# Performance work log

Measured on AMD Instinct MI355X. Metric: run time of the kernel, lower is better.

The kernel has to match this reference:

```python
import jax, jax.numpy as jnp
import numpy as np

N = 16384      # nodes
E = 524288     # edges (avg degree 32)
D = 128        # node_dim
H = 256        # hidden_dim
C = 10         # num_classes
G = 64         # graphs in batch


def setup_inputs() -> dict:
    key = jax.random.key(0)
    ks = jax.random.split(key, 8)
    x = jax.random.normal(ks[0], (N, D), dtype=jnp.float32)
    edge_index = jax.random.randint(ks[1], (2, E), 0, N)
    batch = jnp.sort(jax.random.randint(ks[2], (N,), 0, G))
    s = 0.05
    W1 = jax.random.normal(ks[3], (D, H), dtype=jnp.float32) * s
    b1 = jnp.zeros((H,), dtype=jnp.float32)
    W2 = jax.random.normal(ks[4], (H, H), dtype=jnp.float32) * s
    b2 = jnp.zeros((H,), dtype=jnp.float32)
    Wc = jax.random.normal(ks[5], (H, C), dtype=jnp.float32) * s
    bc = jnp.zeros((C,), dtype=jnp.float32)
    return {"x": x, "edge_index": edge_index, "batch": batch,
            "W1": W1, "b1": b1, "W2": W2, "b2": b2, "Wc": Wc, "bc": bc}


def _adj_norm(edge_index, n, dtype):
    # dense adjacency with self-loops (duplicates collapse to 1 via .set),
    # symmetric degree normalization D^{-1/2} A D^{-1/2}
    adj = jnp.zeros((n, n), dtype=dtype)
    adj = adj.at[edge_index[0], edge_index[1]].set(1.0)
    diag = jnp.arange(n)
    adj = adj.at[diag, diag].set(1.0)
    deg = jnp.clip(adj.sum(axis=1), 1.0, None)
    dis = deg ** -0.5
    return dis[:, None] * adj * dis[None, :]


def reference(x, edge_index, batch, W1, b1, W2, b2, Wc, bc):
    n = x.shape[0]
    A = _adj_norm(edge_index, n, x.dtype)   # [n, n], same for both layers
    h = jax.nn.relu((A @ x) @ W1 + b1)      # GCN layer 1 + relu
    h = jax.nn.relu((A @ h) @ W2 + b2)      # GCN layer 2 + relu
    pooled = jax.ops.segment_sum(h, batch, num_segments=G)            # [G, H]
    counts = jax.ops.segment_sum(jnp.ones((n,), h.dtype), batch, num_segments=G)
    pooled = pooled / jnp.clip(counts, 1.0, None)[:, None]
    # dropout is identity in eval mode
    return pooled @ Wc + bc                  # [G, C]
```

## Files before the change

### kernel.cpp

```cpp
#include <hip/hip_runtime.h>
#include <hip/hip_bf16.h>
#include <hip/hip_fp16.h>

#define NN 16384
#define EE 524288
#define DDIM 128
#define HDIM 256
#define CDIM 10
#define GG 64
#define MAXD 128
#define WPR 512

typedef _Float16 h8 __attribute__((ext_vector_type(8)));
typedef float f4 __attribute__((ext_vector_type(4)));
typedef unsigned short su8 __attribute__((ext_vector_type(8)));

#define OFF_BM   0ull
#define OFF_Y1H  0ull
#define OFF_H1   8388608ull
#define OFF_Y2H  16777216ull
#define OFF_XH   33554432ull
#define OFF_ELL  37748736ull
#define OFF_DIS  41943040ull
#define OFF_DEG  42008576ull
#define OFF_POOL 42074112ull
#define OFF_CNT  42139648ull
#define OFF_WT1  42205184ull
#define OFF_WT2  42270720ull

__global__ void cvt_f16(const float* __restrict__ in, _Float16* __restrict__ out) {
    int i = (blockIdx.x * blockDim.x + threadIdx.x) * 4;
    float4 v = *(const float4*)(in + i);
    _Float16 o[4] = {(_Float16)v.x, (_Float16)v.y, (_Float16)v.z, (_Float16)v.w};
    *(ushort4*)(out + i) = *(ushort4*)o;
}

__global__ void cvt_wt(const float* __restrict__ W, _Float16* __restrict__ Wt, int K) {
    int i = blockIdx.x * 256 + threadIdx.x;
    int n = i / K, k = i - n * K;
    Wt[i] = (_Float16)W[k * 256 + n];
}

__global__ void zero_selfloop(uint4* p) {
    int i = blockIdx.x * blockDim.x + threadIdx.x;
    int stride = gridDim.x * blockDim.x;
    const int n16 = NN * WPR / 4;
    for (; i < n16; i += stride) {
        uint4 z = make_uint4(0u, 0u, 0u, 0u);
        int r = i >> 7;
        int slot = i & 127;
        int sw = r >> 5;
        if ((sw >> 2) == slot) {
            unsigned bit = 1u << (r & 31);
            int comp = sw & 3;
            if (comp == 0) z.x = bit;
            else if (comp == 1) z.y = bit;
            else if (comp == 2) z.z = bit;
            else z.w = bit;
        }
        p[i] = z;
    }
}

__global__ void zero_f(float* p, int n) {
    int i = blockIdx.x * blockDim.x + threadIdx.x;
    if (i < n) p[i] = 0.0f;
}

__global__ void edge_kernel(const int* __restrict__ ei, unsigned* bm) {
    int e = blockIdx.x * blockDim.x + threadIdx.x;
    if (e < EE) {
        int s = ei[e];
        int d = ei[EE + e];
        atomicOr(&bm[s * WPR + (d >> 5)], 1u << (d & 31));
    }
}

__global__ void extract_kernel(const unsigned* __restrict__ bm,
                               unsigned short* __restrict__ ell, int* __restrict__ deg,
                               float* __restrict__ dis) {
    int gtid = blockIdx.x * blockDim.x + threadIdx.x;
    int row  = gtid >> 6;
    int lane = threadIdx.x & 63;
    if (row >= NN) return;
    const uint4* wp = (const uint4*)(bm + (size_t)row * WPR + lane * 8);
    uint4 a = wp[0];
    uint4 b = wp[1];
    unsigned w[8] = {a.x, a.y, a.z, a.w, b.x, b.y, b.z, b.w};
    int pc = 0;
#pragma unroll
    for (int k = 0; k < 8; k++) pc += __popc(w[k]);
    int pre = pc;
#pragma unroll
    for (int off = 1; off < 64; off <<= 1) {
        int o = __shfl_up(pre, off, 64);
        if (lane >= off) pre += o;
    }
    int total = __shfl(pre, 63, 64);
    pre -= pc;
    int base = row * MAXD;
    int pos = pre;
#pragma unroll
    for (int k = 0; k < 8; k++) {
        unsigned bits = w[k];
        int cbase = lane * 256 + k * 32;
        while (bits) {
            int bit = __ffs(bits) - 1;
            if (pos < MAXD) ell[base + pos] = (unsigned short)(cbase + bit);
            pos++;
            bits &= bits - 1;
        }
    }
    if (lane == 0) {
        deg[row] = total < MAXD ? total : MAXD;
        dis[row] = 1.0f / sqrtf((float)total);
    }
}

__global__ __launch_bounds__(256) void spmm_f16(const _Float16* __restrict__ src,
                                                const unsigned short* __restrict__ ell,
                                                const int* __restrict__ deg,
                                                const float* __restrict__ dis,
                                                _Float16* __restrict__ y, int P) {
    __shared__ int2  scw[MAXD];
    __shared__ float red[8][128];
    const int row  = blockIdx.x;
    const int p    = blockIdx.y;
    const int t    = threadIdx.x;
    const int wv   = t >> 6;
    const int lane = t & 63;
    const int half = lane >> 5;
    const int l32  = lane & 31;
    const int d    = deg[row];
    if (t < MAXD) {
        if (t < d) {
            int c = ell[row * MAXD + t];
            scw[t] = make_int2(c, __float_as_int(dis[c]));
        } else {
            scw[t] = make_int2(0, 0);
        }
    }
    __syncthreads();

    const _Float16* plane = src + (size_t)p * NN * 128;
    float a0 = 0.0f, a1 = 0.0f, a2 = 0.0f, a3 = 0.0f;
#pragma unroll 4
    for (int k = wv * 2 + half; k < d; k += 8) {
        int2 pr = scw[k];
        float wgt = __int_as_float(pr.y);
        ushort4 u = *(const ushort4*)(plane + (size_t)pr.x * 128 + l32 * 4);
        _Float16 f0 = *(_Float16*)&u.x, f1 = *(_Float16*)&u.y;
        _Float16 f2 = *(_Float16*)&u.z, f3 = *(_Float16*)&u.w;
        a0 = fmaf(wgt, (float)f0, a0);
        a1 = fmaf(wgt, (float)f1, a1);
        a2 = fmaf(wgt, (float)f2, a2);
        a3 = fmaf(wgt, (float)f3, a3);
    }
    *(float4*)&red[wv * 2 + half][l32 * 4] = make_float4(a0, a1, a2, a3);
    __syncthreads();
    if (t < 128) {
        float s = 0.0f;
#pragma unroll
        for (int q = 0; q < 8; q++) s += red[q][t];
        y[(size_t)row * (P * 128) + p * 128 + t] = (_Float16)(dis[row] * s);
    }
}

#define ASTR 40
#define BSTR 40

#define MFMA_PROLOG                                                            \
    const int r0 = blockIdx.x * 128;                                           \
    const int c0 = blockIdx.y * 64;                                            \
    const int t = threadIdx.x;                                                 \
    const int lane = t & 63, wv = t >> 6;                                      \
    const int wm = wv >> 1, wn = wv & 1;                                       \
    const int qm = lane & 15, qk = lane >> 4;                                  \
    f4 acc[4][2];                                                              \
    _Pragma("unroll") for (int i = 0; i < 4; i++)                              \
        _Pragma("unroll") for (int j = 0; j < 2; j++)                          \
            acc[i][j] = (f4){0.f, 0.f, 0.f, 0.f};

#define MFMA_KLOOP(Aptr, Wtptr, K)                                             \
    for (int k0 = 0; k0 < K; k0 += 32) {                                       \
        __syncthreads();                                                       \
        {                                                                      \
            int r = t >> 1, ko = (t & 1) * 16;                                 \
            const su8* srcA = (const su8*)(Aptr + (size_t)(r0 + r) * K + k0 + ko); \
            su8 a0 = srcA[0], a1 = srcA[1];                                    \
            *(su8*)&As[r * ASTR + ko]     = a0;                                \
            *(su8*)&As[r * ASTR + ko + 8] = a1;                                \
            int n = t >> 2, ko2 = (t & 3) * 8;                                 \
            *(su8*)&Bs[n * BSTR + ko2] =                                       \
                *(const su8*)(Wtptr + (size_t)(c0 + n) * K + k0 + ko2);        \
        }                                                                      \
        __syncthreads();                                                       \
        h8 bfr[2];                                                             \
        _Pragma("unroll") for (int j = 0; j < 2; j++)                          \
            bfr[j] = *(const h8*)&Bs[(wn * 32 + j * 16 + qm) * BSTR + qk * 8]; \
        _Pragma("unroll") for (int i = 0; i < 4; i++) {                        \
            h8 afr = *(const h8*)&As[(wm * 64 + i * 16 + qm) * ASTR + qk * 8]; \
            _Pragma("unroll") for (int j = 0; j < 2; j++)                      \
                acc[i][j] = __builtin_amdgcn_mfma_f32_16x16x32_f16(            \
                    afr, bfr[j], acc[i][j], 0, 0, 0);                          \
        }                                                                      \
    }

template <int K>
__global__ __launch_bounds__(256) void gemm_mfma_f16(
        const _Float16* __restrict__ A, const _Float16* __restrict__ Wt,
        const float* __restrict__ bias, _Float16* __restrict__ H) {
    __shared__ __align__(16) _Float16 As[128 * ASTR];
    __shared__ __align__(16) _Float16 Bs[64 * BSTR];
    __shared__ __align__(16) _Float16 Cs[128 * 72];
    MFMA_PROLOG
    MFMA_KLOOP(A, Wt, K)

    float bv[2];
#pragma unroll
    for (int j = 0; j < 2; j++) bv[j] = bias[c0 + wn * 32 + j * 16 + qm];
#pragma unroll
    for (int i = 0; i < 4; i++)
#pragma unroll
        for (int j = 0; j < 2; j++) {
            int lc = wn * 32 + j * 16 + qm;
#pragma unroll
            for (int rr = 0; rr < 4; rr++) {
                int lr = wm * 64 + i * 16 + qk * 4 + rr;
                Cs[lr * 72 + lc] = (_Float16)fmaxf(acc[i][j][rr] + bv[j], 0.0f);
            }
        }
    __syncthreads();
    {
        int r = t >> 1, half_ = t & 1;
        const int pl = c0 >> 7;
        const int cw = (c0 & 127) + half_ * 32;
        _Float16* dst = H + (size_t)pl * NN * 128 + (size_t)(r0 + r) * 128 + cw;
        const _Float16* srcc = &Cs[r * 72 + half_ * 32];
#pragma unroll
        for (int q = 0; q < 4; q++)
            *(su8*)(dst + q * 8) = *(const su8*)(srcc + q * 8);
    }
}

#define NG 8
template <int K>
__global__ __launch_bounds__(256) void gemm_mfma_pool(
        const _Float16* __restrict__ A, const _Float16* __restrict__ Wt,
        const float* __restrict__ bias, const int* __restrict__ batch,
        float* __restrict__ pooled) {
    __shared__ __align__(16) _Float16 As[128 * ASTR];
    __shared__ __align__(16) _Float16 Bs[64 * BSTR];
    __shared__ float pools[NG][68];
    __shared__ int sb[128];
    MFMA_PROLOG
    if (t < 128) sb[t] = batch[r0 + t];
    for (int i = t; i < NG * 68; i += 256) ((float*)pools)[i] = 0.0f;
    MFMA_KLOOP(A, Wt, K)

    float bv[2];
#pragma unroll
    for (int j = 0; j < 2; j++) bv[j] = bias[c0 + wn * 32 + j * 16 + qm];
    __syncthreads();
    const int g0 = sb[0];
#pragma unroll
    for (int i = 0; i < 4; i++)
#pragma unroll
        for (int j = 0; j < 2; j++) {
            int lc = wn * 32 + j * 16 + qm;
#pragma unroll
            for (int rr = 0; rr < 4; rr++) {
                int lr = wm * 64 + i * 16 + qk * 4 + rr;
                int gi = min(sb[lr] - g0, NG - 1);
                float v = fmaxf(acc[i][j][rr] + bv[j], 0.0f);
                atomicAdd(&pools[gi][lc], v);
            }
        }
    __syncthreads();
    const int ng = min(sb[127] - g0 + 1, NG);
    for (int i2 = t; i2 < ng * 64; i2 += 256) {
        int gi = i2 >> 6, c = i2 & 63;
        float v = pools[gi][c];
        if (v != 0.0f) atomicAdd(&pooled[(g0 + gi) * 256 + c0 + c], v);
    }
}

__global__ void count_kernel(const int* __restrict__ batch, float* cnt) {
    __shared__ int h[GG];
    int t = threadIdx.x;
    if (t < GG) h[t] = 0;
    __syncthreads();
    int i = blockIdx.x * blockDim.x + t;
    if (i < NN) atomicAdd(&h[batch[i]], 1);
    __syncthreads();
    if (t < GG && h[t] > 0) atomicAdd(&cnt[t], (float)h[t]);
}

__global__ void head_kernel(const float* __restrict__ pooled,
                            const float* __restrict__ cnt,
                            const float* __restrict__ Wc,
                            const float* __restrict__ bc,
                            float* __restrict__ out) {
    int g = blockIdx.x;
    int l = threadIdx.x;
    float inv = 1.0f / fmaxf(cnt[g], 1.0f);
    float acc[CDIM];
#pragma unroll
    for (int c = 0; c < CDIM; c++) acc[c] = 0.0f;
    for (int t = l; t < 256; t += 64) {
        float pv = pooled[g * 256 + t] * inv;
#pragma unroll
        for (int c = 0; c < CDIM; c++) acc[c] = fmaf(pv, Wc[t * CDIM + c], acc[c]);
    }
#pragma unroll
    for (int c = 0; c < CDIM; c++) {
        float v = acc[c];
        for (int off = 32; off > 0; off >>= 1) v += __shfl_down(v, off, 64);
        if (l == 0) out[g * CDIM + c] = v + bc[c];
    }
}

extern "C" void kernel_launch(void* const* d_in, const int* in_sizes, int n_in,
                              void* d_out, int out_size, void* d_ws, size_t ws_size,
                              hipStream_t stream) {
    const float* x  = (const float*)d_in[0];
    const int*   ei = (const int*)d_in[1];
    const int*   batch = (const int*)d_in[2];
    const float* W1 = (const float*)d_in[3];
    const float* b1 = (const float*)d_in[4];
    const float* W2 = (const float*)d_in[5];
    const float* b2 = (const float*)d_in[6];
    const float* Wc = (const float*)d_in[7];
    const float* bc = (const float*)d_in[8];
    float* out = (float*)d_out;

    char* ws = (char*)d_ws;
    unsigned* bm   = (unsigned*)(ws + OFF_BM);
    _Float16* y1h  = (_Float16*)(ws + OFF_Y1H);
    _Float16* h1   = (_Float16*)(ws + OFF_H1);
    _Float16* y2h  = (_Float16*)(ws + OFF_Y2H);
    _Float16* xh   = (_Float16*)(ws + OFF_XH);
    unsigned short* ell = (unsigned short*)(ws + OFF_ELL);
    float* dis     = (float*)(ws + OFF_DIS);
    int*   deg     = (int*)(ws + OFF_DEG);
    float* pooled  = (float*)(ws + OFF_POOL);
    float* cnt     = (float*)(ws + OFF_CNT);
    _Float16* wt1  = (_Float16*)(ws + OFF_WT1);
    _Float16* wt2  = (_Float16*)(ws + OFF_WT2);

    cvt_f16<<<(NN * DDIM) / 1024, 256, 0, stream>>>(x, xh);
    cvt_wt<<<(256 * DDIM) / 256, 256, 0, stream>>>(W1, wt1, DDIM);
    cvt_wt<<<(256 * HDIM) / 256, 256, 0, stream>>>(W2, wt2, HDIM);
    zero_selfloop<<<2048, 256, 0, stream>>>((uint4*)bm);
    edge_kernel<<<EE / 256, 256, 0, stream>>>(ei, bm);
    extract_kernel<<<(NN * 64) / 256, 256, 0, stream>>>(bm, ell, deg, dis);
    zero_f<<<(GG * 256 + GG + 255) / 256, 256, 0, stream>>>(pooled, GG * 256 + GG);
    count_kernel<<<NN / 256, 256, 0, stream>>>(batch, cnt);
    {
        dim3 grid(NN, 1);
        spmm_f16<<<grid, 256, 0, stream>>>(xh, ell, deg, dis, y1h, 1);
    }
    {
        dim3 grid(NN / 128, 256 / 64);
        gemm_mfma_f16<DDIM><<<grid, 256, 0, stream>>>(y1h, wt1, b1, h1);
    }
    {
        dim3 grid(NN, 2);
        spmm_f16<<<grid, 256, 0, stream>>>(h1, ell, deg, dis, y2h, 2);
    }
    {
        dim3 grid(NN / 128, 256 / 64);
        gemm_mfma_pool<HDIM><<<grid, 256, 0, stream>>>(y2h, wt2, b2, batch, pooled);
    }
    head_kernel<<<GG, 64, 0, stream>>>(pooled, cnt, Wc, bc, out);
}
```

Measured before the change: 226.9 us.

## Build ELL adjacency via atomic append and warp dedup instead of dense bitmap

```diff
diff --git a/kernel.cpp b/kernel.cpp
--- a/kernel.cpp
+++ b/kernel.cpp
@@ -1,5 +1,4 @@
 #include <hip/hip_runtime.h>
-#include <hip/hip_bf16.h>
 #include <hip/hip_fp16.h>
 
 #define NN 16384
@@ -9,24 +8,23 @@
 #define CDIM 10
 #define GG 64
 #define MAXD 128
-#define WPR 512
 
 typedef _Float16 h8 __attribute__((ext_vector_type(8)));
 typedef float f4 __attribute__((ext_vector_type(4)));
 typedef unsigned short su8 __attribute__((ext_vector_type(8)));
 
-#define OFF_BM   0ull
-#define OFF_Y1H  0ull
-#define OFF_H1   8388608ull
-#define OFF_Y2H  16777216ull
-#define OFF_XH   33554432ull
-#define OFF_ELL  37748736ull
-#define OFF_DIS  41943040ull
-#define OFF_DEG  42008576ull
-#define OFF_POOL 42074112ull
-#define OFF_CNT  42139648ull
-#define OFF_WT1  42205184ull
-#define OFF_WT2  42270720ull
+#define OFF_XH   0ull
+#define OFF_ELL  4194304ull
+#define OFF_ELLW 8388608ull
+#define OFF_Y1H  25165824ull
+#define OFF_H1   29360128ull
+#define OFF_Y2H  37748736ull
+#define OFF_DEG  46137344ull
+#define OFF_DIS  46202880ull
+#define OFF_POOL 46268416ull
+#define OFF_CNT  46333952ull
+#define OFF_WT1  46338048ull
+#define OFF_WT2  46403584ull
 
 __global__ void cvt_f16(const float* __restrict__ in, _Float16* __restrict__ out) {
     int i = (blockIdx.x * blockDim.x + threadIdx.x) * 4;
@@ -41,84 +39,77 @@
     Wt[i] = (_Float16)W[k * 256 + n];
 }
 
-__global__ void zero_selfloop(uint4* p) {
-    int i = blockIdx.x * blockDim.x + threadIdx.x;
-    int stride = gridDim.x * blockDim.x;
-    const int n16 = NN * WPR / 4;
-    for (; i < n16; i += stride) {
-        uint4 z = make_uint4(0u, 0u, 0u, 0u);
-        int r = i >> 7;
-        int slot = i & 127;
-        int sw = r >> 5;
-        if ((sw >> 2) == slot) {
-            unsigned bit = 1u << (r & 31);
-            int comp = sw & 3;
-            if (comp == 0) z.x = bit;
-            else if (comp == 1) z.y = bit;
-            else if (comp == 2) z.z = bit;
-            else z.w = bit;
-        }
-        p[i] = z;
-    }
-}
-
-__global__ void zero_f(float* p, int n) {
-    int i = blockIdx.x * blockDim.x + threadIdx.x;
-    if (i < n) p[i] = 0.0f;
-}
-
-__global__ void edge_kernel(const int* __restrict__ ei, unsigned* bm) {
-    int e = blockIdx.x * blockDim.x + threadIdx.x;
-    if (e < EE) {
-        int s = ei[e];
-        int d = ei[EE + e];
-        atomicOr(&bm[s * WPR + (d >> 5)], 1u << (d & 31));
-    }
-}
-
-__global__ void extract_kernel(const unsigned* __restrict__ bm,
-                               unsigned short* __restrict__ ell, int* __restrict__ deg,
-                               float* __restrict__ dis) {
-    int gtid = blockIdx.x * blockDim.x + threadIdx.x;
-    int row  = gtid >> 6;
+__global__ void init_kernel(unsigned short* __restrict__ ell, int* __restrict__ deg,
+                            float* __restrict__ pooled, float* __restrict__ cnt,
+                            const int* __restrict__ batch) {
+    int r = blockIdx.x * 256 + threadIdx.x;
+    deg[r] = 1;
+    ell[r * MAXD] = (unsigned short)r;
+    pooled[r] = 0.0f;
+    if (r < GG) {
+        int lo = 0, hi = NN;
+        while (lo < hi) { int m = (lo + hi) >> 1; if (batch[m] < r) lo = m + 1; else hi = m; }
+        int a = lo;
+        lo = 0; hi = NN;
+        while (lo < hi) { int m = (lo + hi) >> 1; if (batch[m] < r + 1) lo = m + 1; else hi = m; }
+        cnt[r] = (float)(lo - a);
+    }
+}
+
+__global__ void edge_append(const int* __restrict__ ei, unsigned short* __restrict__ ell,
+                            int* __restrict__ deg) {
+    int e = blockIdx.x * 256 + threadIdx.x;
+    int s = ei[e];
+    int d = ei[EE + e];
+    int pos = atomicAdd(&deg[s], 1);
+    if (pos < MAXD) ell[s * MAXD + pos] = (unsigned short)d;
+}
+
+__global__ __launch_bounds__(256) void dedup_kernel(unsigned short* __restrict__ ell,
+                                                    int* __restrict__ deg,
+                                                    float* __restrict__ dis) {
+    int row  = blockIdx.x * 4 + (threadIdx.x >> 6);
     int lane = threadIdx.x & 63;
-    if (row >= NN) return;
-    const uint4* wp = (const uint4*)(bm + (size_t)row * WPR + lane * 8);
-    uint4 a = wp[0];
-    uint4 b = wp[1];
-    unsigned w[8] = {a.x, a.y, a.z, a.w, b.x, b.y, b.z, b.w};
-    int pc = 0;
-#pragma unroll
-    for (int k = 0; k < 8; k++) pc += __popc(w[k]);
-    int pre = pc;
-#pragma unroll
-    for (int off = 1; off < 64; off <<= 1) {
-        int o = __shfl_up(pre, off, 64);
-        if (lane >= off) pre += o;
-    }
-    int total = __shfl(pre, 63, 64);
-    pre -= pc;
-    int base = row * MAXD;
-    int pos = pre;
-#pragma unroll
-    for (int k = 0; k < 8; k++) {
-        unsigned bits = w[k];
-        int cbase = lane * 256 + k * 32;
-        while (bits) {
-            int bit = __ffs(bits) - 1;
-            if (pos < MAXD) ell[base + pos] = (unsigned short)(cbase + bit);
-            pos++;
-            bits &= bits - 1;
-        }
-    }
+    int d = deg[row];
+    if (d > MAXD) d = MAXD;
+    int c0 = ell[row * MAXD + lane];
+    int c1 = ell[row * MAXD + 64 + lane];
+    bool k0 = lane < d;
+    bool k1 = (64 + lane) < d;
+    for (int j = 0; j < d - 1; j++) {
+        int cj0 = __shfl(c0, j & 63, 64);
+        int cj1 = __shfl(c1, j & 63, 64);
+        int cj = (j < 64) ? cj0 : cj1;
+        if (k0 && lane > j && c0 == cj) k0 = false;
+        if (k1 && (64 + lane) > j && c1 == cj) k1 = false;
+    }
+    unsigned long long m0 = __ballot(k0);
+    unsigned long long m1 = __ballot(k1);
+    int nd = __popcll(m0) + __popcll(m1);
+    unsigned long long below = (lane == 0) ? 0ull : ((~0ull) >> (64 - lane));
+    int p0 = __popcll(m0 & below);
+    int p1 = __popcll(m0) + __popcll(m1 & below);
+    if (k0) ell[row * MAXD + p0] = (unsigned short)c0;
+    if (k1) ell[row * MAXD + p1] = (unsigned short)c1;
     if (lane == 0) {
-        deg[row] = total < MAXD ? total : MAXD;
-        dis[row] = 1.0f / sqrtf((float)total);
-    }
+        deg[row] = nd;
+        dis[row] = 1.0f / sqrtf((float)nd);
+    }
+}
+
+__global__ void well_kernel(const unsigned short* __restrict__ ell,
+                            const int* __restrict__ deg, const float* __restrict__ dis,
+                            int2* __restrict__ ellw) {
+    int i = blockIdx.x * 256 + threadIdx.x;
+    int row = i >> 7;
+    int slot = i & 127;
+    int c = ell[i];
+    float w = (slot < deg[row]) ? dis[c] : 0.0f;
+    ellw[i] = make_int2(c, __float_as_int(w));
 }
 
 __global__ __launch_bounds__(256) void spmm_f16(const _Float16* __restrict__ src,
-                                                const unsigned short* __restrict__ ell,
+                                                const int2* __restrict__ ellw,
                                                 const int* __restrict__ deg,
                                                 const float* __restrict__ dis,
                                                 _Float16* __restrict__ y, int P) {
@@ -132,14 +123,7 @@
     const int half = lane >> 5;
     const int l32  = lane & 31;
     const int d    = deg[row];
-    if (t < MAXD) {
-        if (t < d) {
-            int c = ell[row * MAXD + t];
-            scw[t] = make_int2(c, __float_as_int(dis[c]));
-        } else {
-            scw[t] = make_int2(0, 0);
-        }
-    }
+    if (t < MAXD) scw[t] = ellw[row * MAXD + t];
     __syncthreads();
 
     const _Float16* plane = src + (size_t)p * NN * 128;
@@ -285,17 +269,6 @@
     }
 }
 
-__global__ void count_kernel(const int* __restrict__ batch, float* cnt) {
-    __shared__ int h[GG];
-    int t = threadIdx.x;
-    if (t < GG) h[t] = 0;
-    __syncthreads();
-    int i = blockIdx.x * blockDim.x + t;
-    if (i < NN) atomicAdd(&h[batch[i]], 1);
-    __syncthreads();
-    if (t < GG && h[t] > 0) atomicAdd(&cnt[t], (float)h[t]);
-}
-
 __global__ void head_kernel(const float* __restrict__ pooled,
                             const float* __restrict__ cnt,
                             const float* __restrict__ Wc,
@@ -335,14 +308,14 @@
     float* out = (float*)d_out;
 
     char* ws = (char*)d_ws;
-    unsigned* bm   = (unsigned*)(ws + OFF_BM);
+    _Float16* xh   = (_Float16*)(ws + OFF_XH);
+    unsigned short* ell = (unsigned short*)(ws + OFF_ELL);
+    int2* ellw     = (int2*)(ws + OFF_ELLW);
     _Float16* y1h  = (_Float16*)(ws + OFF_Y1H);
     _Float16* h1   = (_Float16*)(ws + OFF_H1);
     _Float16* y2h  = (_Float16*)(ws + OFF_Y2H);
-    _Float16* xh   = (_Float16*)(ws + OFF_XH);
-    unsigned short* ell = (unsigned short*)(ws + OFF_ELL);
+    int*   deg     = (int*)(ws + OFF_DEG);
     float* dis     = (float*)(ws + OFF_DIS);
-    int*   deg     = (int*)(ws + OFF_DEG);
     float* pooled  = (float*)(ws + OFF_POOL);
     float* cnt     = (float*)(ws + OFF_CNT);
     _Float16* wt1  = (_Float16*)(ws + OFF_WT1);
@@ -351,14 +324,13 @@
     cvt_f16<<<(NN * DDIM) / 1024, 256, 0, stream>>>(x, xh);
     cvt_wt<<<(256 * DDIM) / 256, 256, 0, stream>>>(W1, wt1, DDIM);
     cvt_wt<<<(256 * HDIM) / 256, 256, 0, stream>>>(W2, wt2, HDIM);
-    zero_selfloop<<<2048, 256, 0, stream>>>((uint4*)bm);
-    edge_kernel<<<EE / 256, 256, 0, stream>>>(ei, bm);
-    extract_kernel<<<(NN * 64) / 256, 256, 0, stream>>>(bm, ell, deg, dis);
-    zero_f<<<(GG * 256 + GG + 255) / 256, 256, 0, stream>>>(pooled, GG * 256 + GG);
-    count_kernel<<<NN / 256, 256, 0, stream>>>(batch, cnt);
+    init_kernel<<<NN / 256, 256, 0, stream>>>(ell, deg, pooled, cnt, batch);
+    edge_append<<<EE / 256, 256, 0, stream>>>(ei, ell, deg);
+    dedup_kernel<<<NN / 4, 256, 0, stream>>>(ell, deg, dis);
+    well_kernel<<<(NN * MAXD) / 256, 256, 0, stream>>>(ell, deg, dis, ellw);
     {
         dim3 grid(NN, 1);
-        spmm_f16<<<grid, 256, 0, stream>>>(xh, ell, deg, dis, y1h, 1);
+        spmm_f16<<<grid, 256, 0, stream>>>(xh, ellw, deg, dis, y1h, 1);
     }
     {
         dim3 grid(NN / 128, 256 / 64);
@@ -366,7 +338,7 @@
     }
     {
         dim3 grid(NN, 2);
-        spmm_f16<<<grid, 256, 0, stream>>>(h1, ell, deg, dis, y2h, 2);
+        spmm_f16<<<grid, 256, 0, stream>>>(h1, ellw, deg, dis, y2h, 2);
     }
     {
         dim3 grid(NN / 128, 256 / 64);
```

Measured after the change: 240.1 us. 5.8% more time.
